# Performance work log

Hardware: AMD Instinct MI355X
Metric: run time of the kernel (lower is better)

## Reference

```python
import jax, jax.numpy as jnp
import numpy as np

N_NEURONS = 50000
N_BKG = 100
N_SYN_BASIS = 5
N_EDGES = 500000
BATCH = 1
SEQ_T = 250
BKG_RATE_PROB = 0.25  # bkg_firing_rate(250) * 0.001


def setup_inputs() -> dict:
    key = jax.random.key(0)
    k_w, k_tau, k_sp, k_r, k_c = jax.random.split(key, 5)
    weights = jax.random.normal(k_w, (N_EDGES,), dtype=jnp.float32)
    tau_syn = jax.random.uniform(k_tau, (N_EDGES, N_SYN_BASIS), dtype=jnp.float32)
    # Bernoulli background spikes, shape [B*T, n_bkg_units]
    spikes = (jax.random.uniform(k_sp, (BATCH * SEQ_T, N_BKG)) < BKG_RATE_PROB).astype(jnp.float32)
    rows = jax.random.randint(k_r, (N_EDGES,), 0, N_NEURONS, dtype=jnp.int32)
    cols = jax.random.randint(k_c, (N_EDGES,), 0, N_BKG, dtype=jnp.int32)
    return {"weights": weights, "tau_syn": tau_syn, "spikes": spikes,
            "rows": rows, "cols": cols}


def reference(weights, tau_syn, spikes, rows, cols):
    # Per-receptor edge values: weights[e] * tau_syn[e, r]  -> [E, R]
    vals = weights[:, None] * tau_syn
    # Densify the (identical-structure) sparse matrix once for all receptors;
    # duplicate (row, col) indices accumulate, matching tf.sparse semantics
    # used through sparse_dense_matmul. W: [N, K, R]
    W = jnp.zeros((N_NEURONS, N_BKG, N_SYN_BASIS), dtype=spikes.dtype).at[rows, cols].add(vals)
    # i_receptor[r] = sparse_w_in @ spikes.T -> stacked [R, N, BT];
    # tf.transpose reverses axes -> [BT, N, R]; fused here as one einsum.
    out = jnp.einsum('nkr,bk->bnr', W, spikes)  # [BT, N, R]
    return out.reshape(BATCH, SEQ_T, N_NEURONS * N_SYN_BASIS)
```

## Files before the change

kernel.cpp:

```cpp
#include <hip/hip_runtime.h>


#define N_NEURONS 50000
#define N_BKG     100
#define N_SYN     5
#define N_EDGES   500000
#define SEQ_T     250
#define NCOL      (N_NEURONS * N_SYN)
#define RPB       16
#define NBINS     (N_NEURONS / RPB)
#define CAP       512
#define REC_U32   4
#define KPAD      128
#define CPAD      80
#define BCOLS     80
#define LDS_BYTES 32000

#define WS_COUNT_OFF 0
#define WS_SPB_OFF   32768
#define WS_REC_OFF   131072

typedef __attribute__((ext_vector_type(8))) short bf16x8;
typedef __attribute__((ext_vector_type(4))) float f32x4;

__device__ inline unsigned short bf16_rne(float f) {
    unsigned u = __builtin_bit_cast(unsigned, f);
    u += 0x7FFFu + ((u >> 16) & 1u);
    return (unsigned short)(u >> 16);
}
__device__ inline float bf16_up(unsigned hw) {
    return __builtin_bit_cast(float, hw << 16);
}

__global__ __launch_bounds__(256) void bucket_kernel(
        const float* __restrict__ weights,
        const float* __restrict__ tau,
        const int*   __restrict__ rows,
        const int*   __restrict__ cols,
        const float* __restrict__ spikes,
        unsigned* __restrict__ count,
        uint4* __restrict__ rec,
        unsigned short* __restrict__ spb) {
    int gid = blockIdx.x * 256 + threadIdx.x;
    if (gid < 256 * KPAD) {
        int t = gid >> 7, k = gid & 127;
        unsigned short v = 0;
        if (t < SEQ_T && k < N_BKG) {
            float s = spikes[t * N_BKG + k];
            v = bf16_rne(s);
        }
        spb[gid] = v;
    }
    if (gid >= N_EDGES) return;
    int row = rows[gid];
    int col = cols[gid];
    float w = weights[gid];
    const float* tp = tau + (size_t)gid * N_SYN;
    int bin = row >> 4;
    unsigned slot = atomicAdd(&count[bin], 1u);
    if (slot >= CAP) return;
    uint4 r;
    r.x = ((unsigned)col << 4) | (unsigned)(row & 15);
    r.y = (unsigned)bf16_rne(w * tp[0]) | ((unsigned)bf16_rne(w * tp[1]) << 16);
    r.z = (unsigned)bf16_rne(w * tp[2]) | ((unsigned)bf16_rne(w * tp[3]) << 16);
    r.w = (unsigned)bf16_rne(w * tp[4]);
    rec[(size_t)bin * CAP + slot] = r;
}

__global__ __launch_bounds__(256, 4) void fused_kernel(
        const unsigned* __restrict__ count,
        const uint4* __restrict__ rec,
        const unsigned short* __restrict__ spb,
        float* __restrict__ out) {
    __shared__ __align__(16) char lds[LDS_BYTES];
    float* slice = (float*)lds;

    const int tid = threadIdx.x;
    const int b   = blockIdx.x;

    unsigned cnt = count[b];
    if (cnt > CAP) cnt = CAP;
    uint4 ra, rb;
    bool havea = (unsigned)tid < cnt;
    bool haveb = (unsigned)(tid + 256) < cnt;
    if (havea) ra = rec[(size_t)b * CAP + tid];
    if (haveb) rb = rec[(size_t)b * CAP + tid + 256];

    {
        float4* s4 = (float4*)slice;
        float4 z = make_float4(0.f, 0.f, 0.f, 0.f);
#pragma unroll
        for (int j = 0; j < 8; ++j) {
            int i = tid + j * 256;
            if (i < 2000) s4[i] = z;
        }
    }
    __syncthreads();

    if (havea) {
        float* base = &slice[(ra.x >> 4) * CPAD + (ra.x & 15u) * N_SYN];
        atomicAdd(base + 0, bf16_up(ra.y & 0xFFFFu));
        atomicAdd(base + 1, bf16_up(ra.y >> 16));
        atomicAdd(base + 2, bf16_up(ra.z & 0xFFFFu));
        atomicAdd(base + 3, bf16_up(ra.z >> 16));
        atomicAdd(base + 4, bf16_up(ra.w & 0xFFFFu));
    }
    if (haveb) {
        float* base = &slice[(rb.x >> 4) * CPAD + (rb.x & 15u) * N_SYN];
        atomicAdd(base + 0, bf16_up(rb.y & 0xFFFFu));
        atomicAdd(base + 1, bf16_up(rb.y >> 16));
        atomicAdd(base + 2, bf16_up(rb.z & 0xFFFFu));
        atomicAdd(base + 3, bf16_up(rb.z >> 16));
        atomicAdd(base + 4, bf16_up(rb.w & 0xFFFFu));
    }
    __syncthreads();

    bf16x8 hi[5];
    unsigned bo[5];
#pragma unroll
    for (int j = 0; j < 5; ++j) {
        int m  = tid + j * 256;
        int c  = m % BCOLS;
        int kb = m / BCOLS;
#pragma unroll
        for (int i = 0; i < 8; ++i) {
            int k = kb * 8 + i;
            float v = (k < N_BKG) ? slice[k * CPAD + c] : 0.f;
            hi[j][i] = (short)bf16_rne(v);
        }
        bo[j] = (unsigned)((c * 256 + kb * 16) ^ ((c & 7) << 4));
    }
    __syncthreads();
#pragma unroll
    for (int j = 0; j < 5; ++j)
        *(bf16x8*)(lds + bo[j]) = hi[j];
    __syncthreads();

    const int l  = tid & 63;
    const int wv = tid >> 6;
    const int lc = l & 15;
    const int lq = l >> 4;

    f32x4 acc[5][4];
#pragma unroll
    for (int m = 0; m < 5; ++m)
#pragma unroll
        for (int n = 0; n < 4; ++n)
            acc[m][n] = (f32x4){0.f, 0.f, 0.f, 0.f};

#pragma unroll
    for (int kk = 0; kk < 4; ++kk) {
        bf16x8 bs[4];
#pragma unroll
        for (int n = 0; n < 4; ++n) {
            int t = (wv * 4 + n) * 16 + lc;
            bs[n] = *(const bf16x8*)(spb + (size_t)t * KPAD + kk * 32 + lq * 8);
        }
#pragma unroll
        for (int m = 0; m < 5; ++m) {
            int c = m * 16 + lc;
            unsigned bor = (unsigned)((c * 256 + kk * 64 + lq * 16) ^ ((c & 7) << 4));
            bf16x8 ah = *(const bf16x8*)(lds + bor);
#pragma unroll
            for (int n = 0; n < 4; ++n)
                acc[m][n] = __builtin_amdgcn_mfma_f32_16x16x32_bf16(
                                ah, bs[n], acc[m][n], 0, 0, 0);
        }
    }

    const int cb = b * BCOLS;
#pragma unroll
    for (int m = 0; m < 5; ++m) {
        int c = cb + m * 16 + lq * 4;
#pragma unroll
        for (int n = 0; n < 4; ++n) {
            int t = (wv * 4 + n) * 16 + lc;
            if (t < SEQ_T)
                *(f32x4*)(out + (size_t)t * NCOL + c) = acc[m][n];
        }
    }
}

extern "C" void kernel_launch(void* const* d_in, const int* in_sizes, int n_in,
                              void* d_out, int out_size, void* d_ws, size_t ws_size,
                              hipStream_t stream) {
    const float* weights = (const float*)d_in[0];
    const float* tau     = (const float*)d_in[1];
    const float* spikes  = (const float*)d_in[2];
    const int*   rows    = (const int*)d_in[3];
    const int*   cols    = (const int*)d_in[4];
    float* out = (float*)d_out;

    char* ws = (char*)d_ws;
    unsigned*       count = (unsigned*)(ws + WS_COUNT_OFF);
    unsigned short* spb   = (unsigned short*)(ws + WS_SPB_OFF);
    uint4*          rec   = (uint4*)(ws + WS_REC_OFF);

    hipMemsetAsync(count, 0, NBINS * sizeof(unsigned), stream);

    int eblocks = (N_EDGES + 255) / 256;
    bucket_kernel<<<eblocks, 256, 0, stream>>>(weights, tau, rows, cols, spikes,
                                               count, rec, spb);

    fused_kernel<<<NBINS, 256, 0, stream>>>(count, rec, spb, out);
}
```

Measured before the change: 123.4 us.

## Split fused kernel into scatter and MFMA-fragment-layout GEMM kernels

Splits the fused scatter-plus-GEMM kernel in two. The scatter kernel accumulates each bin's weights in LDS, with the row pitch padded from 80 to 81 floats to reduce bank conflicts, and writes bf16 operands to global memory already arranged in MFMA fragment order. The spike matrix is also pre-packed in fragment order, so the GEMM kernel loads both operands with plain coalesced vector reads and uses no LDS or barriers, which lets the GEMM run at higher occupancy. In exchange it adds a third launch and a global round trip of the dense weight tiles (about 3125 x 20 KB), and record loads are now unconditional.

```diff
diff --git a/kernel.cpp b/kernel.cpp
--- a/kernel.cpp
+++ b/kernel.cpp
@@ -10,15 +10,14 @@
 #define RPB       16
 #define NBINS     (N_NEURONS / RPB)
 #define CAP       512
-#define REC_U32   4
 #define KPAD      128
-#define CPAD      80
+#define CPAD      81
 #define BCOLS     80
-#define LDS_BYTES 32000
 
 #define WS_COUNT_OFF 0
 #define WS_SPB_OFF   32768
 #define WS_REC_OFF   131072
+#define WS_WG_OFF    (131072 + (size_t)NBINS * CAP * 16)
 
 typedef __attribute__((ext_vector_type(8))) short bf16x8;
 typedef __attribute__((ext_vector_type(4))) float f32x4;
@@ -40,16 +39,23 @@
         const float* __restrict__ spikes,
         unsigned* __restrict__ count,
         uint4* __restrict__ rec,
-        unsigned short* __restrict__ spb) {
+        bf16x8* __restrict__ spbf) {
     int gid = blockIdx.x * 256 + threadIdx.x;
-    if (gid < 256 * KPAD) {
-        int t = gid >> 7, k = gid & 127;
-        unsigned short v = 0;
-        if (t < SEQ_T && k < N_BKG) {
-            float s = spikes[t * N_BKG + k];
-            v = bf16_rne(s);
-        }
-        spb[gid] = v;
+    if (gid < 4096) {
+        int lane = gid & 63;
+        int kk   = (gid >> 6) & 3;
+        int nt   = gid >> 8;
+        int t    = nt * 16 + (lane & 15);
+        int k0   = kk * 32 + (lane >> 4) * 8;
+        bf16x8 v;
+#pragma unroll
+        for (int i = 0; i < 8; ++i) {
+            float s = 0.f;
+            if (t < SEQ_T && (k0 + i) < N_BKG)
+                s = spikes[t * N_BKG + k0 + i];
+            v[i] = (short)bf16_rne(s);
+        }
+        spbf[gid] = v;
     }
     if (gid >= N_EDGES) return;
     int row = rows[gid];
@@ -67,37 +73,32 @@
     rec[(size_t)bin * CAP + slot] = r;
 }
 
-__global__ __launch_bounds__(256, 4) void fused_kernel(
+__global__ __launch_bounds__(256, 4) void scatter_kernel(
         const unsigned* __restrict__ count,
         const uint4* __restrict__ rec,
-        const unsigned short* __restrict__ spb,
-        float* __restrict__ out) {
-    __shared__ __align__(16) char lds[LDS_BYTES];
-    float* slice = (float*)lds;
+        bf16x8* __restrict__ wg) {
+    __shared__ float slice[N_BKG * CPAD];
 
     const int tid = threadIdx.x;
     const int b   = blockIdx.x;
 
     unsigned cnt = count[b];
+    uint4 ra = rec[(size_t)b * CAP + tid];
+    uint4 rb = rec[(size_t)b * CAP + tid + 256];
     if (cnt > CAP) cnt = CAP;
-    uint4 ra, rb;
-    bool havea = (unsigned)tid < cnt;
-    bool haveb = (unsigned)(tid + 256) < cnt;
-    if (havea) ra = rec[(size_t)b * CAP + tid];
-    if (haveb) rb = rec[(size_t)b * CAP + tid + 256];
 
     {
-        float4* s4 = (float4*)slice;
-        float4 z = make_float4(0.f, 0.f, 0.f, 0.f);
+        f32x4* s4 = (f32x4*)slice;
+        f32x4 z = (f32x4){0.f, 0.f, 0.f, 0.f};
 #pragma unroll
         for (int j = 0; j < 8; ++j) {
             int i = tid + j * 256;
-            if (i < 2000) s4[i] = z;
+            if (i < 2025) s4[i] = z;
         }
     }
     __syncthreads();
 
-    if (havea) {
+    if ((unsigned)tid < cnt) {
         float* base = &slice[(ra.x >> 4) * CPAD + (ra.x & 15u) * N_SYN];
         atomicAdd(base + 0, bf16_up(ra.y & 0xFFFFu));
         atomicAdd(base + 1, bf16_up(ra.y >> 16));
@@ -105,7 +106,7 @@
         atomicAdd(base + 3, bf16_up(ra.z >> 16));
         atomicAdd(base + 4, bf16_up(ra.w & 0xFFFFu));
     }
-    if (haveb) {
+    if ((unsigned)tid + 256u < cnt) {
         float* base = &slice[(rb.x >> 4) * CPAD + (rb.x & 15u) * N_SYN];
         atomicAdd(base + 0, bf16_up(rb.y & 0xFFFFu));
         atomicAdd(base + 1, bf16_up(rb.y >> 16));
@@ -115,32 +116,39 @@
     }
     __syncthreads();
 
-    bf16x8 hi[5];
-    unsigned bo[5];
+    bf16x8* wgb = wg + (size_t)b * 1280;
 #pragma unroll
     for (int j = 0; j < 5; ++j) {
-        int m  = tid + j * 256;
-        int c  = m % BCOLS;
-        int kb = m / BCOLS;
+        int u    = j * 256 + tid;
+        int kk   = u / 320;
+        int rem  = u - kk * 320;
+        int m    = rem >> 6;
+        int lane = rem & 63;
+        int c    = m * 16 + (lane & 15);
+        int k0   = kk * 32 + (lane >> 4) * 8;
+        bf16x8 v;
 #pragma unroll
         for (int i = 0; i < 8; ++i) {
-            int k = kb * 8 + i;
-            float v = (k < N_BKG) ? slice[k * CPAD + c] : 0.f;
-            hi[j][i] = (short)bf16_rne(v);
-        }
-        bo[j] = (unsigned)((c * 256 + kb * 16) ^ ((c & 7) << 4));
-    }
-    __syncthreads();
-#pragma unroll
-    for (int j = 0; j < 5; ++j)
-        *(bf16x8*)(lds + bo[j]) = hi[j];
-    __syncthreads();
-
+            float f = (k0 + i < N_BKG) ? slice[(k0 + i) * CPAD + c] : 0.f;
+            v[i] = (short)bf16_rne(f);
+        }
+        wgb[(kk * 5 + m) * 64 + lane] = v;
+    }
+}
+
+__global__ __launch_bounds__(256, 4) void gemm_kernel(
+        const bf16x8* __restrict__ wg,
+        const bf16x8* __restrict__ spbf,
+        float* __restrict__ out) {
+    const int tid = threadIdx.x;
+    const int b   = blockIdx.x;
     const int l  = tid & 63;
     const int wv = tid >> 6;
     const int lc = l & 15;
     const int lq = l >> 4;
 
+    const bf16x8* wgb = wg + (size_t)b * 1280;
+
     f32x4 acc[5][4];
 #pragma unroll
     for (int m = 0; m < 5; ++m)
@@ -153,14 +161,12 @@
         bf16x8 bs[4];
 #pragma unroll
         for (int n = 0; n < 4; ++n) {
-            int t = (wv * 4 + n) * 16 + lc;
-            bs[n] = *(const bf16x8*)(spb + (size_t)t * KPAD + kk * 32 + lq * 8);
+            int nt = wv * 4 + n;
+            bs[n] = spbf[(nt * 4 + kk) * 64 + l];
         }
 #pragma unroll
         for (int m = 0; m < 5; ++m) {
-            int c = m * 16 + lc;
-            unsigned bor = (unsigned)((c * 256 + kk * 64 + lq * 16) ^ ((c & 7) << 4));
-            bf16x8 ah = *(const bf16x8*)(lds + bor);
+            bf16x8 ah = wgb[(kk * 5 + m) * 64 + l];
 #pragma unroll
             for (int n = 0; n < 4; ++n)
                 acc[m][n] = __builtin_amdgcn_mfma_f32_16x16x32_bf16(
@@ -192,15 +198,18 @@
     float* out = (float*)d_out;
 
     char* ws = (char*)d_ws;
-    unsigned*       count = (unsigned*)(ws + WS_COUNT_OFF);
-    unsigned short* spb   = (unsigned short*)(ws + WS_SPB_OFF);
-    uint4*          rec   = (uint4*)(ws + WS_REC_OFF);
+    unsigned* count = (unsigned*)(ws + WS_COUNT_OFF);
+    bf16x8*   spbf  = (bf16x8*)(ws + WS_SPB_OFF);
+    uint4*    rec   = (uint4*)(ws + WS_REC_OFF);
+    bf16x8*   wg    = (bf16x8*)(ws + WS_WG_OFF);
 
     hipMemsetAsync(count, 0, NBINS * sizeof(unsigned), stream);
 
     int eblocks = (N_EDGES + 255) / 256;
     bucket_kernel<<<eblocks, 256, 0, stream>>>(weights, tau, rows, cols, spikes,
-                                               count, rec, spb);
-
-    fused_kernel<<<NBINS, 256, 0, stream>>>(count, rec, spb, out);
-}
+                                               count, rec, spbf);
+
+    scatter_kernel<<<NBINS, 256, 0, stream>>>(count, rec, wg);
+
+    gemm_kernel<<<NBINS, 256, 0, stream>>>(wg, spbf, out);
+}
```

Result: slower. 157.8 us (+27.8%).
